# Performance work log

Measured on AMD Instinct MI355X. Metric: run time of the kernel, lower is better.

The kernel has to match this reference:

```python
import jax, jax.numpy as jnp
import numpy as np

B = 32           # graphs in batch
N_PER = 512      # nodes per graph
N = B * N_PER    # 16384 total nodes (block-diagonal batched graph)
E = N * 16       # 262144 edges
D_IN = 128
D_OUT = 128
ASSIGN = 2048    # total clusters = B * K
K = ASSIGN // B  # 64 clusters per graph


def setup_inputs() -> dict:
    key = jax.random.key(0)
    ks = jax.random.split(key, 6)
    h = jax.random.normal(ks[0], (N, D_IN), jnp.float32)
    # edges confined within each graph -> block-diagonal batched adjacency
    gid = jnp.repeat(jnp.arange(B), E // B)
    edge_src = (jax.random.randint(ks[1], (E,), 0, N_PER) + gid * N_PER).astype(jnp.int32)
    edge_dst = (jax.random.randint(ks[2], (E,), 0, N_PER) + gid * N_PER).astype(jnp.int32)
    # GraphSage NodeApply linears: Linear(2*in, out)
    stdv_f = 1.0 / np.sqrt(2 * D_IN)
    W_feat = jax.random.uniform(ks[3], (2 * D_IN, D_OUT), jnp.float32, -stdv_f, stdv_f)
    b_feat = jnp.zeros((D_OUT,), jnp.float32)
    W_pool = jax.random.uniform(ks[4], (2 * D_IN, ASSIGN), jnp.float32, -stdv_f, stdv_f)
    b_pool = jnp.zeros((ASSIGN,), jnp.float32)
    return {"h": h, "W_feat": W_feat, "b_feat": b_feat,
            "W_pool": W_pool, "b_pool": b_pool,
            "edge_src": edge_src, "edge_dst": edge_dst}


def _graphsage(h, W, b, src, dst):
    # mean aggregation over in-neighbors (dropout=0, batch_norm off)
    msg = jax.ops.segment_sum(h[src], dst, num_segments=N)          # [N, d_in]
    deg = jax.ops.segment_sum(jnp.ones((src.shape[0],), h.dtype), dst, num_segments=N)
    h_neigh = msg / jnp.maximum(deg, 1.0)[:, None]
    bundle = jnp.concatenate([h, h_neigh], axis=1) @ W + b          # [N, d_out]
    # F.normalize(p=2, dim=1) then activation, as in GraphSage NodeApply
    norm = jnp.linalg.norm(bundle, axis=1, keepdims=True)
    bundle = bundle / jnp.maximum(norm, 1e-12)
    return jax.nn.relu(bundle)


def _forward(h, W_feat, b_feat, W_pool, b_pool, src, dst):
    feat = _graphsage(h, W_feat, b_feat, src, dst)       # [N, D_OUT]
    assign = _graphsage(h, W_pool, b_pool, src, dst)     # [N, ASSIGN]
    # block-diagonal mask: node i of graph g may only assign to g's K clusters
    gid_n = jnp.arange(N) // N_PER                       # [N]
    gid_c = jnp.arange(ASSIGN) // K                      # [ASSIGN]
    mask = (gid_n[:, None] == gid_c[None, :]).astype(jnp.float32)
    # masked_softmax with memory_efficient=False
    s = jax.nn.softmax(assign * mask, axis=-1) * mask
    s = s / (s.sum(axis=-1, keepdims=True) + 1e-13)      # [N, ASSIGN]
    h_new = s.T @ feat                                   # [ASSIGN, D_OUT]
    # adj_new = S^T A S without densifying A: (A S)[dst] += S[src]
    a_s = jax.ops.segment_sum(s[src], dst, num_segments=N)
    adj_new = s.T @ a_s                                  # [ASSIGN, ASSIGN]
    return adj_new, h_new


def reference(h, W_feat, b_feat, W_pool, b_pool, edge_src, edge_dst):
    return _forward(h, W_feat, b_feat, W_pool, b_pool, edge_src, edge_dst)
```

## Files before the change

### kernel.cpp

```cpp
#include <hip/hip_runtime.h>

#define NB   32
#define NPER 512
#define NN   16384
#define EE   262144
#define DD   128
#define AS   2048
#define KC   64

using short8   = __attribute__((ext_vector_type(8))) short;
using floatx4  = __attribute__((ext_vector_type(4))) float;
using ushort4v = __attribute__((ext_vector_type(4))) unsigned short;

typedef __attribute__((address_space(3))) unsigned int lds_u32;
typedef const __attribute__((address_space(1))) unsigned int gbl_u32;

static __device__ __forceinline__ void gload16(const unsigned short* g, unsigned short* l) {
    __builtin_amdgcn_global_load_lds((gbl_u32*)g, (lds_u32*)l, 16, 0, 0);
}
static __device__ __forceinline__ float bits2f(unsigned int u) {
    union { unsigned int i; float f; } z; z.i = u << 16; return z.f;
}
static __device__ __forceinline__ unsigned short f2b(float x) {
    union { float f; unsigned int u; } v; v.f = x;
    unsigned int r = v.u + 0x7fffu + ((v.u >> 16) & 1u);
    return (unsigned short)(r >> 16);
}
static __device__ __forceinline__ unsigned short f2b_exact(float x) {
    union { float f; unsigned int u; } v; v.f = x;
    return (unsigned short)(v.u >> 16);
}

union PrepSMem {
    unsigned short fT[128 * 136];
    float tl[32][33];
    struct { unsigned short glA[4096]; unsigned short glB[4096]; float gcred[4]; } gg;
};
__global__ void prep_kernel(const float* __restrict__ h, unsigned short* __restrict__ bundle,
                            unsigned short* __restrict__ hT, const int* __restrict__ esrc,
                            const int* __restrict__ edst, unsigned int* __restrict__ Acnt,
                            const float* __restrict__ Wf, const float* __restrict__ Wp,
                            const float* __restrict__ bp,
                            unsigned short* __restrict__ WfT, unsigned short* __restrict__ WpT,
                            float* __restrict__ Gf, float* __restrict__ uF,
                            float* __restrict__ cF) {
    __shared__ PrepSMem sm;
    int b = blockIdx.x, t = threadIdx.x;
    if (b < 32) {
        int ks = b >> 2, ti = (b >> 1) & 1, tj = b & 1;
        int wv = t >> 6, lane = t & 63;
        int mw = wv >> 1, nw = wv & 1, q = lane >> 4, lm = lane & 15;
        int swz = q ^ ((lm >> 1) & 3);
        floatx4 acc[4][4];
#pragma unroll
        for (int mi = 0; mi < 4; mi++)
#pragma unroll
            for (int ni = 0; ni < 4; ni++) acc[mi][ni] = (floatx4)0.f;
        for (int ki = 0; ki < 8; ki++) {
            int k0 = ks * 256 + ki * 32;
#pragma unroll
            for (int half = 0; half < 2; half++) {
                int u = t + 256 * half;
                int row = u >> 2, c = u & 3;
                int cs = c ^ ((row >> 1) & 3);
                const float4* sa = reinterpret_cast<const float4*>(
                    Wp + (size_t)(ti * 128 + row) * 2048 + k0 + c * 8);
                float4 v0 = sa[0], v1 = sa[1];
                ushort4v p0 = { f2b(v0.x), f2b(v0.y), f2b(v0.z), f2b(v0.w) };
                ushort4v p1 = { f2b(v1.x), f2b(v1.y), f2b(v1.z), f2b(v1.w) };
                *reinterpret_cast<ushort4v*>(&sm.gg.glA[(row * 4 + cs) * 8]) = p0;
                *reinterpret_cast<ushort4v*>(&sm.gg.glA[(row * 4 + cs) * 8 + 4]) = p1;
                const float4* sb = reinterpret_cast<const float4*>(
                    Wp + (size_t)(tj * 128 + row) * 2048 + k0 + c * 8);
                float4 w0 = sb[0], w1 = sb[1];
                ushort4v q0 = { f2b(w0.x), f2b(w0.y), f2b(w0.z), f2b(w0.w) };
                ushort4v q1 = { f2b(w1.x), f2b(w1.y), f2b(w1.z), f2b(w1.w) };
                *reinterpret_cast<ushort4v*>(&sm.gg.glB[(row * 4 + cs) * 8]) = q0;
                *reinterpret_cast<ushort4v*>(&sm.gg.glB[(row * 4 + cs) * 8 + 4]) = q1;
            }
            __syncthreads();
            short8 aF[4], bF[4];
#pragma unroll
            for (int mi = 0; mi < 4; mi++)
                aF[mi] = *reinterpret_cast<const short8*>(&sm.gg.glA[((64 * mw + 16 * mi + lm) * 4 + swz) * 8]);
#pragma unroll
            for (int ni = 0; ni < 4; ni++)
                bF[ni] = *reinterpret_cast<const short8*>(&sm.gg.glB[((64 * nw + 16 * ni + lm) * 4 + swz) * 8]);
#pragma unroll
            for (int mi = 0; mi < 4; mi++)
#pragma unroll
                for (int ni = 0; ni < 4; ni++)
                    acc[mi][ni] = __builtin_amdgcn_mfma_f32_16x16x32_bf16(aF[mi], bF[ni], acc[mi][ni], 0, 0, 0);
            __syncthreads();
        }
#pragma unroll
        for (int mi = 0; mi < 4; mi++)
#pragma unroll
            for (int ni = 0; ni < 4; ni++)
#pragma unroll
                for (int r = 0; r < 4; r++)
                    atomicAdd(&Gf[(size_t)(ti * 128 + 64 * mw + 16 * mi + 4 * q + r) * 256 +
                                  tj * 128 + 64 * nw + 16 * ni + lm], acc[mi][ni][r]);
        if (tj == 0) {
            int row = t >> 1, jh = t & 1;
            const float4* wr = reinterpret_cast<const float4*>(
                Wp + (size_t)(ti * 128 + row) * 2048 + ks * 256 + jh * 128);
            const float4* br = reinterpret_cast<const float4*>(bp + ks * 256 + jh * 128);
            float s = 0.f;
#pragma unroll 8
            for (int j = 0; j < 32; j++) {
                float4 a = wr[j], c = br[j];
                s += a.x * c.x + a.y * c.y + a.z * c.z + a.w * c.w;
            }
            s += __shfl_xor(s, 1, 64);
            if (jh == 0) atomicAdd(&uF[ti * 128 + row], s);
        }
        if (b == 0) {
            float s = 0.f;
            for (int j = t; j < 2048; j += 256) { float v = bp[j]; s += v * v; }
#pragma unroll
            for (int d = 1; d < 64; d <<= 1) s += __shfl_xor(s, d, 64);
            if (lane == 0) sm.gg.gcred[wv] = s;
            __syncthreads();
            if (t == 0) atomicAdd(cF, sm.gg.gcred[0] + sm.gg.gcred[1] + sm.gg.gcred[2] + sm.gg.gcred[3]);
        }
    } else if (b < 160) {
        int node0 = (b - 32) * 128;
        int r = t >> 1, hf = t & 1;
        const float4* h4 = reinterpret_cast<const float4*>(h + (size_t)(node0 + r) * 128 + hf * 64);
        unsigned short* bo = bundle + (size_t)(node0 + r) * 256 + hf * 64;
#pragma unroll
        for (int i = 0; i < 16; i++) {
            float4 v = h4[i];
            ushort4v o = { f2b(v.x), f2b(v.y), f2b(v.z), f2b(v.w) };
            *reinterpret_cast<ushort4v*>(bo + 4 * i) = o;
            int c = hf * 64 + 4 * i;
            sm.fT[(c + 0) * 136 + r] = o.x;
            sm.fT[(c + 1) * 136 + r] = o.y;
            sm.fT[(c + 2) * 136 + r] = o.z;
            sm.fT[(c + 3) * 136 + r] = o.w;
        }
        __syncthreads();
        int c = t >> 1, nh = t & 1;
        const uint4* src = reinterpret_cast<const uint4*>(&sm.fT[c * 136 + nh * 64]);
        uint4* dst = reinterpret_cast<uint4*>(hT + (size_t)c * NN + node0 + nh * 64);
#pragma unroll
        for (int i = 0; i < 8; i++) dst[i] = src[i];
    } else if (b < 1184) {
        int e = (b - 160) * 256 + t;
        int d = edst[e], sl = esrc[e] & 511;
        int idx = d * 512 + sl;
        atomicAdd(&Acnt[idx >> 2], 1u << (8 * (idx & 3)));
    } else {
        int tb = b - 1184;
        int bx = tb % 68, by = tb / 68;
        int tx = t & 31, ty = t >> 5;
        const float* in; unsigned short* out; int C, cb;
        if (bx < DD / 32) { in = Wf; out = WfT; C = DD; cb = bx; }
        else              { in = Wp; out = WpT; C = AS; cb = bx - DD / 32; }
        int c0 = cb * 32, r0 = by * 32;
        for (int i = 0; i < 4; i++)
            sm.tl[ty + 8 * i][tx] = in[(size_t)(r0 + ty + 8 * i) * C + c0 + tx];
        __syncthreads();
        for (int i = 0; i < 4; i++)
            out[(size_t)(c0 + ty + 8 * i) * 256 + r0 + tx] = f2b(sm.tl[tx][ty + 8 * i]);
    }
}

__global__ __launch_bounds__(256) void agg_h_mfma_kernel(
    const unsigned int* __restrict__ Acnt, const unsigned short* __restrict__ hT,
    unsigned short* __restrict__ bundle, unsigned short* __restrict__ Aadj,
    const float* __restrict__ Gf, unsigned short* __restrict__ Gb) {
    __shared__ alignas(16) unsigned short lA[64 * 512];
    __shared__ float rs[64];
    int tid = threadIdx.x, bx = blockIdx.x;
    if (bx >= 256) {
        int base = (bx - 256) * 16384;
        for (int i = 0; i < 16; i++) {
            int idx = base + i * 1024 + tid * 4;
            float4 v = *reinterpret_cast<const float4*>(Gf + idx);
            ushort4v o = { f2b(v.x), f2b(v.y), f2b(v.z), f2b(v.w) };
            *reinterpret_cast<ushort4v*>(&Gb[idx]) = o;
        }
        return;
    }
    int r0 = bx * 64, g = bx >> 3;
    int wv = tid >> 6, lane = tid & 63, q = lane >> 4, lm = lane & 15;
    int mw = wv >> 1, nw = wv & 1;
    if (tid < 64) rs[tid] = 0.f;
    __syncthreads();
#pragma unroll
    for (int j = 0; j < 8; j++) {
        int ub = tid + 256 * j;
        int row = ub >> 5, kb = ub & 31;
        uint4 w = reinterpret_cast<const uint4*>(Acnt)[(size_t)(r0 + row) * 32 + kb];
        unsigned int wa[4] = { w.x, w.y, w.z, w.w };
        unsigned short ob[16];
        float sum = 0.f;
#pragma unroll
        for (int i = 0; i < 4; i++) {
#pragma unroll
            for (int bb = 0; bb < 4; bb++) {
                float fv = (float)((wa[i] >> (8 * bb)) & 0xffu);
                sum += fv;
                ob[4 * i + bb] = f2b_exact(fv);
            }
        }
        atomicAdd(&rs[row], sum);
        uint4* gdst = reinterpret_cast<uint4*>(&Aadj[(size_t)(r0 + row) * 512 + kb * 16]);
        gdst[0] = *reinterpret_cast<const uint4*>(&ob[0]);
        gdst[1] = *reinterpret_cast<const uint4*>(&ob[8]);
#pragma unroll
        for (int jj = 0; jj < 2; jj++) {
            int pos = (kb * 2 + jj) ^ (row & 7);
            *reinterpret_cast<uint4*>(&lA[(row * 64 + pos) * 8]) =
                *reinterpret_cast<const uint4*>(&ob[8 * jj]);
        }
    }
    floatx4 acc[2][4];
#pragma unroll
    for (int mt = 0; mt < 2; mt++)
#pragma unroll
        for (int nt = 0; nt < 4; nt++) acc[mt][nt] = (floatx4)0.f;
    __syncthreads();
    const unsigned short* Bb = hT + (size_t)(64 * nw + lm) * NN + g * 512 + (q << 3);
    short8 bF[2][4];
#pragma unroll
    for (int nt = 0; nt < 4; nt++)
        bF[0][nt] = *reinterpret_cast<const short8*>(Bb + (size_t)16 * nt * NN);
    for (int ki = 0; ki < 16; ki++) {
        if (ki < 15) {
#pragma unroll
            for (int nt = 0; nt < 4; nt++)
                bF[(ki + 1) & 1][nt] =
                    *reinterpret_cast<const short8*>(Bb + (size_t)16 * nt * NN + (ki + 1) * 32);
        }
        short8 aF[2];
        int swz = (4 * ki + q) ^ (lm & 7);
#pragma unroll
        for (int mt = 0; mt < 2; mt++)
            aF[mt] = *reinterpret_cast<const short8*>(&lA[((32 * mw + 16 * mt + lm) * 64 + swz) * 8]);
#pragma unroll
        for (int mt = 0; mt < 2; mt++)
#pragma unroll
            for (int nt = 0; nt < 4; nt++)
                acc[mt][nt] = __builtin_amdgcn_mfma_f32_16x16x32_bf16(aF[mt], bF[ki & 1][nt],
                                                                      acc[mt][nt], 0, 0, 0);
    }
#pragma unroll
    for (int mt = 0; mt < 2; mt++)
#pragma unroll
        for (int r = 0; r < 4; r++) {
            int row = 32 * mw + 16 * mt + 4 * q + r;
            float inv = 1.0f / fmaxf(rs[row], 1.0f);
#pragma unroll
            for (int nt = 0; nt < 4; nt++)
                bundle[(size_t)(r0 + row) * 256 + 128 + 64 * nw + 16 * nt + lm] =
                    f2b(acc[mt][nt][r] * inv);
        }
}

union FPSMem {
    struct { unsigned short lA[4096]; unsigned short lB[4096]; float red[256]; } feat;
    struct { unsigned short lA[16384]; float raw[4352]; float ssq[256]; float rn[64];
             float uL[256]; } pool;
};
__global__ __launch_bounds__(256) void featpool_kernel(
    const unsigned short* __restrict__ bundle, const unsigned short* __restrict__ WfT,
    const unsigned short* __restrict__ WpT, const unsigned short* __restrict__ Gb,
    const float* __restrict__ bfe, const float* __restrict__ bp,
    const float* __restrict__ uF, const float* __restrict__ cF,
    unsigned short* __restrict__ featT, unsigned short* __restrict__ sT) {
    __shared__ FPSMem sm;
    int tid = threadIdx.x, b = blockIdx.x;
    if (b < 128) {
        int r0 = b * 128;
        int wv = tid >> 6, lane = tid & 63;
        int mw = wv >> 1, nw = wv & 1, q = lane >> 4, lm = lane & 15;
        int rowS0 = tid >> 2,         cS0 = (tid & 3) ^ ((rowS0 >> 1) & 3);
        int rowS1 = (tid + 256) >> 2, cS1 = ((tid + 256) & 3) ^ ((rowS1 >> 1) & 3);
        int swz = q ^ ((lm >> 1) & 3);
        floatx4 acc[4][4];
#pragma unroll
        for (int mi = 0; mi < 4; mi++)
#pragma unroll
            for (int ni = 0; ni < 4; ni++) acc[mi][ni] = (floatx4)0.f;
        for (int k0 = 0; k0 < 256; k0 += 32) {
            gload16(bundle + (size_t)(r0 + rowS0) * 256 + k0 + 8 * cS0, &sm.feat.lA[tid * 8]);
            gload16(bundle + (size_t)(r0 + rowS1) * 256 + k0 + 8 * cS1, &sm.feat.lA[(tid + 256) * 8]);
            gload16(WfT + (size_t)rowS0 * 256 + k0 + 8 * cS0, &sm.feat.lB[tid * 8]);
            gload16(WfT + (size_t)rowS1 * 256 + k0 + 8 * cS1, &sm.feat.lB[(tid + 256) * 8]);
            __syncthreads();
            short8 aF[4], bF[4];
#pragma unroll
            for (int mi = 0; mi < 4; mi++)
                aF[mi] = *reinterpret_cast<const short8*>(&sm.feat.lA[((64 * mw + 16 * mi + lm) * 4 + swz) * 8]);
#pragma unroll
            for (int ni = 0; ni < 4; ni++)
                bF[ni] = *reinterpret_cast<const short8*>(&sm.feat.lB[((64 * nw + 16 * ni + lm) * 4 + swz) * 8]);
#pragma unroll
            for (int mi = 0; mi < 4; mi++)
#pragma unroll
                for (int ni = 0; ni < 4; ni++)
                    acc[mi][ni] = __builtin_amdgcn_mfma_f32_16x16x32_bf16(aF[mi], bF[ni], acc[mi][ni], 0, 0, 0);
            __syncthreads();
        }
#pragma unroll
        for (int ni = 0; ni < 4; ni++) {
            float bv = bfe[64 * nw + 16 * ni + lm];
#pragma unroll
            for (int mi = 0; mi < 4; mi++)
#pragma unroll
                for (int r = 0; r < 4; r++) acc[mi][ni][r] += bv;
        }
#pragma unroll
        for (int mi = 0; mi < 4; mi++)
#pragma unroll
            for (int r = 0; r < 4; r++) {
                float p = 0.f;
#pragma unroll
                for (int ni = 0; ni < 4; ni++) p += acc[mi][ni][r] * acc[mi][ni][r];
                p += __shfl_xor(p, 1, 64);
                p += __shfl_xor(p, 2, 64);
                p += __shfl_xor(p, 4, 64);
                p += __shfl_xor(p, 8, 64);
                if (lm == 0) sm.feat.red[nw * 128 + 64 * mw + 16 * mi + 4 * q + r] = p;
            }
        __syncthreads();
#pragma unroll
        for (int mi = 0; mi < 4; mi++) {
            float rrn[4];
#pragma unroll
            for (int r = 0; r < 4; r++) {
                int rl = 64 * mw + 16 * mi + 4 * q + r;
                rrn[r] = 1.0f / fmaxf(sqrtf(sm.feat.red[rl] + sm.feat.red[128 + rl]), 1e-12f);
            }
#pragma unroll
            for (int ni = 0; ni < 4; ni++) {
                int col = 64 * nw + 16 * ni + lm;
                ushort4v pk = { f2b(fmaxf(acc[mi][ni][0] * rrn[0], 0.f)),
                                f2b(fmaxf(acc[mi][ni][1] * rrn[1], 0.f)),
                                f2b(fmaxf(acc[mi][ni][2] * rrn[2], 0.f)),
                                f2b(fmaxf(acc[mi][ni][3] * rrn[3], 0.f)) };
                *reinterpret_cast<ushort4v*>(
                    &featT[(size_t)col * NN + r0 + 64 * mw + 16 * mi + 4 * q]) = pk;
            }
        }
    } else {
        int bx = b - 128;
        int r0 = bx * 64, g = bx >> 3;
        int wv = tid >> 6, lane = tid & 63, q = lane >> 4, lm = lane & 15;
#pragma unroll
        for (int j = 0; j < 8; j++) {
            int u = tid + 256 * j;
            int row = u >> 5;
            int chunk = (u & 31) ^ (row & 7);
            gload16(bundle + (size_t)(r0 + row) * 256 + chunk * 8, &sm.pool.lA[u * 8]);
        }
        sm.pool.uL[tid] = uF[tid];
        __syncthreads();
        {
            const unsigned short* Bb = Gb + ((size_t)(wv * 64 + lm) << 8) + (q << 3);
            short8 bF[2][4];
#pragma unroll
            for (int ni = 0; ni < 4; ni++)
                bF[0][ni] = *reinterpret_cast<const short8*>(Bb + (ni << 12));
            floatx4 acc[4][4];
#pragma unroll
            for (int mi = 0; mi < 4; mi++)
#pragma unroll
                for (int ni = 0; ni < 4; ni++) acc[mi][ni] = (floatx4)0.f;
#pragma unroll
            for (int k = 0; k < 8; k++) {
                if (k < 7) {
#pragma unroll
                    for (int ni = 0; ni < 4; ni++)
                        bF[(k + 1) & 1][ni] =
                            *reinterpret_cast<const short8*>(Bb + (ni << 12) + ((k + 1) << 5));
                }
                short8 aF[4];
                int swz = (4 * k + q) ^ (lm & 7);
#pragma unroll
                for (int mi = 0; mi < 4; mi++)
                    aF[mi] = *reinterpret_cast<const short8*>(&sm.pool.lA[((16 * mi + lm) * 32 + swz) * 8]);
#pragma unroll
                for (int mi = 0; mi < 4; mi++)
#pragma unroll
                    for (int ni = 0; ni < 4; ni++)
                        acc[mi][ni] = __builtin_amdgcn_mfma_f32_16x16x32_bf16(aF[mi], bF[k & 1][ni],
                                                                              acc[mi][ni], 0, 0, 0);
            }
            float uc[4];
#pragma unroll
            for (int ni = 0; ni < 4; ni++) uc[ni] = sm.pool.uL[64 * wv + 16 * ni + lm];
#pragma unroll
            for (int mi = 0; mi < 4; mi++)
#pragma unroll
                for (int r = 0; r < 4; r++) {
                    int row = 16 * mi + 4 * q + r;
                    float p = 0.f;
#pragma unroll
                    for (int ni = 0; ni < 4; ni++) {
                        int col = 64 * wv + 16 * ni + lm;
                        int cu = (col >> 3) ^ (row & 7);
                        float xv = bits2f((unsigned int)sm.pool.lA[(row * 32 + cu) * 8 + (col & 7)]);
                        p += (acc[mi][ni][r] + 2.f * uc[ni]) * xv;
                    }
                    p += __shfl_xor(p, 1, 64);
                    p += __shfl_xor(p, 2, 64);
                    p += __shfl_xor(p, 4, 64);
                    p += __shfl_xor(p, 8, 64);
                    if (lm == 0) sm.pool.ssq[wv * 64 + row] = p;
                }
        }
        {
            const unsigned short* Bb2 = WpT + (size_t)(g * KC + 16 * wv + lm) * 256 + (q << 3);
            short8 b2[2];
            b2[0] = *reinterpret_cast<const short8*>(Bb2);
            floatx4 acc2[4];
#pragma unroll
            for (int mi = 0; mi < 4; mi++) acc2[mi] = (floatx4)0.f;
#pragma unroll
            for (int k = 0; k < 8; k++) {
                if (k < 7) b2[(k + 1) & 1] = *reinterpret_cast<const short8*>(Bb2 + ((k + 1) << 5));
                short8 aF[4];
                int swz = (4 * k + q) ^ (lm & 7);
#pragma unroll
                for (int mi = 0; mi < 4; mi++)
                    aF[mi] = *reinterpret_cast<const short8*>(&sm.pool.lA[((16 * mi + lm) * 32 + swz) * 8]);
#pragma unroll
                for (int mi = 0; mi < 4; mi++)
                    acc2[mi] = __builtin_amdgcn_mfma_f32_16x16x32_bf16(aF[mi], b2[k & 1], acc2[mi], 0, 0, 0);
            }
            float bv = bp[g * KC + 16 * wv + lm];
#pragma unroll
            for (int mi = 0; mi < 4; mi++)
#pragma unroll
                for (int r = 0; r < 4; r++)
                    sm.pool.raw[(16 * mi + 4 * q + r) * 68 + 16 * wv + lm] = acc2[mi][r] + bv;
        }
        __syncthreads();
        if (tid < 64)
            sm.pool.rn[tid] = 1.0f / fmaxf(sqrtf(sm.pool.ssq[tid] + sm.pool.ssq[64 + tid] +
                                           sm.pool.ssq[128 + tid] + sm.pool.ssq[192 + tid] + cF[0]), 1e-12f);
        __syncthreads();
        {
            int row = tid >> 2, j = tid & 3;
            int nloc = ((bx & 7) << 6) + row;
            float rn = sm.pool.rn[row];
            float v[16];
            float mx = -1e30f;
#pragma unroll
            for (int c4 = 0; c4 < 4; c4++) {
                float4 rv = *reinterpret_cast<const float4*>(&sm.pool.raw[row * 68 + 16 * j + 4 * c4]);
                v[4 * c4 + 0] = fmaxf(rv.x * rn, 0.f);
                v[4 * c4 + 1] = fmaxf(rv.y * rn, 0.f);
                v[4 * c4 + 2] = fmaxf(rv.z * rn, 0.f);
                v[4 * c4 + 3] = fmaxf(rv.w * rn, 0.f);
            }
#pragma unroll
            for (int c = 0; c < 16; c++) mx = fmaxf(mx, v[c]);
            mx = fmaxf(mx, __shfl_xor(mx, 1, 64));
            mx = fmaxf(mx, __shfl_xor(mx, 2, 64));
            float z = 0.f;
#pragma unroll
            for (int c = 0; c < 16; c++) { v[c] = __expf(v[c] - mx); z += v[c]; }
            z += __shfl_xor(z, 1, 64);
            z += __shfl_xor(z, 2, 64);
            float iz = 1.0f / z;
#pragma unroll
            for (int c4 = 0; c4 < 4; c4++) {
                size_t tb = (size_t)(g * KC + 16 * j + 4 * c4) * NPER + nloc;
                sT[tb] = f2b(v[4 * c4 + 0] * iz);
                sT[tb + NPER] = f2b(v[4 * c4 + 1] * iz);
                sT[tb + 2 * NPER] = f2b(v[4 * c4 + 2] * iz);
                sT[tb + 3 * NPER] = f2b(v[4 * c4 + 3] * iz);
            }
        }
    }
}

__global__ __launch_bounds__(256) void as_mfma_kernel(
    const unsigned short* __restrict__ sT, const unsigned short* __restrict__ Aadj,
    unsigned short* __restrict__ asT) {
    __shared__ alignas(16) unsigned short lS[64 * 512];
    int tid = threadIdx.x, bx = blockIdx.x;
    int g = bx >> 1, half = bx & 1;
    int wv = tid >> 6, lane = tid & 63, q = lane >> 4, lm = lane & 15;
#pragma unroll
    for (int j = 0; j < 16; j++) {
        int u = tid + 256 * j;
        int row = u >> 6, cu = (u & 63) ^ (row & 7);
        gload16(sT + (size_t)(g * KC + row) * NPER + cu * 8, &lS[u * 8]);
    }
    floatx4 acc[4][4];
#pragma unroll
    for (int mi = 0; mi < 4; mi++)
#pragma unroll
        for (int nt = 0; nt < 4; nt++) acc[mi][nt] = (floatx4)0.f;
    __syncthreads();
    int dbase = half * 256 + wv * 64;
    const unsigned short* Bb = Aadj + (size_t)(g * 512 + dbase + lm) * 512 + (q << 3);
    short8 bF[2][4];
#pragma unroll
    for (int nt = 0; nt < 4; nt++)
        bF[0][nt] = *reinterpret_cast<const short8*>(Bb + (size_t)16 * nt * 512);
    for (int ki = 0; ki < 16; ki++) {
        if (ki < 15) {
#pragma unroll
            for (int nt = 0; nt < 4; nt++)
                bF[(ki + 1) & 1][nt] =
                    *reinterpret_cast<const short8*>(Bb + (size_t)16 * nt * 512 + (ki + 1) * 32);
        }
        short8 aF[4];
        int swz = (4 * ki + q) ^ (lm & 7);
#pragma unroll
        for (int mi = 0; mi < 4; mi++)
            aF[mi] = *reinterpret_cast<const short8*>(&lS[((16 * mi + lm) * 64 + swz) * 8]);
#pragma unroll
        for (int mi = 0; mi < 4; mi++)
#pragma unroll
            for (int nt = 0; nt < 4; nt++)
                acc[mi][nt] = __builtin_amdgcn_mfma_f32_16x16x32_bf16(aF[mi], bF[ki & 1][nt],
                                                                      acc[mi][nt], 0, 0, 0);
    }
#pragma unroll
    for (int mi = 0; mi < 4; mi++)
#pragma unroll
        for (int r = 0; r < 4; r++) {
            int row = 16 * mi + 4 * q + r;
#pragma unroll
            for (int nt = 0; nt < 4; nt++)
                asT[(size_t)(g * KC + row) * NPER + dbase + 16 * nt + lm] = f2b(acc[mi][nt][r]);
        }
}

__global__ __launch_bounds__(256) void hnew_adj2_kernel(
    const unsigned short* __restrict__ sT, const unsigned short* __restrict__ featT,
    const unsigned short* __restrict__ asT, float* __restrict__ adjf,
    float* __restrict__ hnewf) {
    __shared__ alignas(16) unsigned short lS[1024 * 8];
    __shared__ alignas(16) unsigned short lF[2048 * 8];
    __shared__ alignas(16) unsigned short lAS[1024 * 8];
    int tid = threadIdx.x, b = blockIdx.x;
    if (b >= 32) {
        uint4 z = { 0u, 0u, 0u, 0u };
        for (int row = b - 32; row < AS; row += 224) {
            int g = row >> 6;
            uint4* out = reinterpret_cast<uint4*>(adjf + (size_t)row * AS);
            for (int i = tid; i < 512; i += 256)
                if (i < g * 16 || i >= g * 16 + 16) out[i] = z;
        }
        return;
    }
    int g = b;
    int wv = tid >> 6, lane = tid & 63, q = lane >> 4, lm = lane & 15;
    bool isH = (wv < 2);
    floatx4 accH[4][4];
    floatx4 accA[4][2];
#pragma unroll
    for (int mi = 0; mi < 4; mi++) {
#pragma unroll
        for (int ni = 0; ni < 4; ni++) accH[mi][ni] = (floatx4)0.f;
#pragma unroll
        for (int ni = 0; ni < 2; ni++) accA[mi][ni] = (floatx4)0.f;
    }
    for (int ks = 0; ks < 4; ks++) {
#pragma unroll
        for (int j = 0; j < 4; j++) {
            int u = tid + 256 * j;
            int row = u >> 4, cu = (u & 15) ^ (row & 15);
            gload16(sT + (size_t)(g * KC + row) * NPER + ks * 128 + cu * 8, &lS[u * 8]);
        }
#pragma unroll
        for (int j = 0; j < 8; j++) {
            int u = tid + 256 * j;
            int row = u >> 4, cu = (u & 15) ^ (row & 15);
            gload16(featT + (size_t)row * NN + g * NPER + ks * 128 + cu * 8, &lF[u * 8]);
        }
#pragma unroll
        for (int j = 0; j < 4; j++) {
            int u = tid + 256 * j;
            int row = u >> 4, cu = (u & 15) ^ (row & 15);
            gload16(asT + (size_t)(g * KC + row) * NPER + ks * 128 + cu * 8, &lAS[u * 8]);
        }
        __syncthreads();
#pragma unroll
        for (int kk = 0; kk < 4; kk++) {
            short8 aF[4];
#pragma unroll
            for (int mi = 0; mi < 4; mi++)
                aF[mi] = *reinterpret_cast<const short8*>(
                    &lS[((16 * mi + lm) * 16 + ((4 * kk + q) ^ lm)) * 8]);
            if (isH) {
                short8 bF[4];
#pragma unroll
                for (int ni = 0; ni < 4; ni++)
                    bF[ni] = *reinterpret_cast<const short8*>(
                        &lF[((64 * wv + 16 * ni + lm) * 16 + ((4 * kk + q) ^ lm)) * 8]);
#pragma unroll
                for (int mi = 0; mi < 4; mi++)
#pragma unroll
                    for (int ni = 0; ni < 4; ni++)
                        accH[mi][ni] = __builtin_amdgcn_mfma_f32_16x16x32_bf16(aF[mi], bF[ni],
                                                                               accH[mi][ni], 0, 0, 0);
            } else {
                short8 bF[2];
#pragma unroll
                for (int ni = 0; ni < 2; ni++)
                    bF[ni] = *reinterpret_cast<const short8*>(
                        &lAS[((32 * (wv - 2) + 16 * ni + lm) * 16 + ((4 * kk + q) ^ lm)) * 8]);
#pragma unroll
                for (int mi = 0; mi < 4; mi++)
#pragma unroll
                    for (int ni = 0; ni < 2; ni++)
                        accA[mi][ni] = __builtin_amdgcn_mfma_f32_16x16x32_bf16(aF[mi], bF[ni],
                                                                               accA[mi][ni], 0, 0, 0);
            }
        }
        __syncthreads();
    }
    if (isH) {
#pragma unroll
        for (int mi = 0; mi < 4; mi++)
#pragma unroll
            for (int ni = 0; ni < 4; ni++)
#pragma unroll
                for (int r = 0; r < 4; r++)
                    hnewf[(size_t)(g * KC + 16 * mi + 4 * q + r) * DD +
                          64 * wv + 16 * ni + lm] = accH[mi][ni][r];
    } else {
#pragma unroll
        for (int mi = 0; mi < 4; mi++)
#pragma unroll
            for (int ni = 0; ni < 2; ni++)
#pragma unroll
                for (int r = 0; r < 4; r++)
                    adjf[(size_t)(g * KC + 16 * mi + 4 * q + r) * AS +
                         g * KC + 32 * (wv - 2) + 16 * ni + lm] = accA[mi][ni][r];
    }
}

extern "C" void kernel_launch(void* const* d_in, const int* in_sizes, int n_in,
                              void* d_out, int out_size, void* d_ws, size_t ws_size,
                              hipStream_t stream) {
    const float* h   = (const float*)d_in[0];
    const float* Wf  = (const float*)d_in[1];
    const float* bfe = (const float*)d_in[2];
    const float* Wp  = (const float*)d_in[3];
    const float* bp  = (const float*)d_in[4];
    const int* esrc  = (const int*)d_in[5];
    const int* edst  = (const int*)d_in[6];

    float* adjf  = (float*)d_out;
    float* hnewf = adjf + (size_t)AS * AS;

    unsigned short* bundle = (unsigned short*)d_ws;
    unsigned short* WfT   = bundle + (size_t)NN * 256;
    unsigned short* WpT   = WfT + 128 * 256;
    unsigned short* sT    = WpT + (size_t)AS * 256;
    unsigned short* asT   = sT + (size_t)NN * KC;
    unsigned short* featT = asT + (size_t)NN * KC;
    unsigned short* hT    = featT + (size_t)DD * NN;
    unsigned short* Aadj  = hT + (size_t)DD * NN;
    unsigned int* Acnt = (unsigned int*)(Aadj + (size_t)NN * 512);
    float* Gf = (float*)(Acnt + (size_t)NN * 128);
    float* uF = Gf + 65536;
    float* cF = uF + 256;
    unsigned short* Gb = (unsigned short*)(cF + 4);

    hipMemsetAsync(Acnt, 0, (size_t)NN * 512 + (65536 + 256 + 4) * sizeof(float), stream);

    prep_kernel<<<1728, 256, 0, stream>>>(h, bundle, hT, esrc, edst, Acnt,
                                          Wf, Wp, bp, WfT, WpT, Gf, uF, cF);
    agg_h_mfma_kernel<<<260, 256, 0, stream>>>(Acnt, hT, bundle, Aadj, Gf, Gb);
    featpool_kernel<<<384, 256, 0, stream>>>(bundle, WfT, WpT, Gb, bfe, bp, uF, cF, featT, sT);
    as_mfma_kernel<<<NB * 2, 256, 0, stream>>>(sT, Aadj, asT);
    hnew_adj2_kernel<<<256, 256, 0, stream>>>(sT, featT, asT, adjf, hnewf);
}
```

Baseline: 162.9 us.

## Fuse neighbor aggregation, feature linear and pool softmax into one mid kernel

Merges the aggregation MFMA kernel and the feat/pool linear kernel into a single per-64-row block kernel. The aggregated half of each bundle row stays in LDS instead of round-tripping through global memory. The Gram matrix is converted to bf16 in registers on the fly, which removes the separate Gf-to-Gb conversion blocks. Row degree sums now use wave shuffles instead of LDS atomics. The cost is fewer blocks (256 instead of 384+260) with a larger LDS footprint, and serialized phases per block, which may lower occupancy and parallelism.

```diff
diff --git a/kernel.cpp b/kernel.cpp
--- a/kernel.cpp
+++ b/kernel.cpp
@@ -1,4 +1,5 @@
 #include <hip/hip_runtime.h>
+#include <hip/hip_bf16.h>
 
 #define NB   32
 #define NPER 512
@@ -29,6 +30,18 @@
 static __device__ __forceinline__ unsigned short f2b_exact(float x) {
     union { float f; unsigned int u; } v; v.f = x;
     return (unsigned short)(v.u >> 16);
+}
+static __device__ __forceinline__ short8 pk8(float4 a, float4 b) {
+    union { short8 s; unsigned int u[4]; } o;
+    __hip_bfloat162 t0 = __float22bfloat162_rn(make_float2(a.x, a.y));
+    __hip_bfloat162 t1 = __float22bfloat162_rn(make_float2(a.z, a.w));
+    __hip_bfloat162 t2 = __float22bfloat162_rn(make_float2(b.x, b.y));
+    __hip_bfloat162 t3 = __float22bfloat162_rn(make_float2(b.z, b.w));
+    o.u[0] = *reinterpret_cast<unsigned int*>(&t0);
+    o.u[1] = *reinterpret_cast<unsigned int*>(&t1);
+    o.u[2] = *reinterpret_cast<unsigned int*>(&t2);
+    o.u[3] = *reinterpret_cast<unsigned int*>(&t3);
+    return o.s;
 }
 
 union PrepSMem {
@@ -167,28 +180,33 @@
     }
 }
 
-__global__ __launch_bounds__(256) void agg_h_mfma_kernel(
+union MSMem {
+    unsigned short lA[64 * 512];
+    struct {
+        unsigned short tile[64 * 256];
+        float rs[64];
+        float raw[64 * 68];
+        float ssq[256];
+        float rn[64];
+        float uL[256];
+        float red[256];
+        float rn2[64];
+    } p;
+};
+__global__ __launch_bounds__(256) void fused_mid_kernel(
     const unsigned int* __restrict__ Acnt, const unsigned short* __restrict__ hT,
-    unsigned short* __restrict__ bundle, unsigned short* __restrict__ Aadj,
-    const float* __restrict__ Gf, unsigned short* __restrict__ Gb) {
-    __shared__ alignas(16) unsigned short lA[64 * 512];
-    __shared__ float rs[64];
+    const unsigned short* __restrict__ bundle, unsigned short* __restrict__ Aadj,
+    const float* __restrict__ Gf, const unsigned short* __restrict__ WpT,
+    const unsigned short* __restrict__ WfT, const float* __restrict__ bfe,
+    const float* __restrict__ bp, const float* __restrict__ uF, const float* __restrict__ cF,
+    unsigned short* __restrict__ featT, unsigned short* __restrict__ sT) {
+    __shared__ MSMem sm;
     int tid = threadIdx.x, bx = blockIdx.x;
-    if (bx >= 256) {
-        int base = (bx - 256) * 16384;
-        for (int i = 0; i < 16; i++) {
-            int idx = base + i * 1024 + tid * 4;
-            float4 v = *reinterpret_cast<const float4*>(Gf + idx);
-            ushort4v o = { f2b(v.x), f2b(v.y), f2b(v.z), f2b(v.w) };
-            *reinterpret_cast<ushort4v*>(&Gb[idx]) = o;
-        }
-        return;
-    }
     int r0 = bx * 64, g = bx >> 3;
     int wv = tid >> 6, lane = tid & 63, q = lane >> 4, lm = lane & 15;
     int mw = wv >> 1, nw = wv & 1;
-    if (tid < 64) rs[tid] = 0.f;
-    __syncthreads();
+
+    float rsum[8];
 #pragma unroll
     for (int j = 0; j < 8; j++) {
         int ub = tid + 256 * j;
@@ -206,16 +224,21 @@
                 ob[4 * i + bb] = f2b_exact(fv);
             }
         }
-        atomicAdd(&rs[row], sum);
         uint4* gdst = reinterpret_cast<uint4*>(&Aadj[(size_t)(r0 + row) * 512 + kb * 16]);
         gdst[0] = *reinterpret_cast<const uint4*>(&ob[0]);
         gdst[1] = *reinterpret_cast<const uint4*>(&ob[8]);
 #pragma unroll
         for (int jj = 0; jj < 2; jj++) {
             int pos = (kb * 2 + jj) ^ (row & 7);
-            *reinterpret_cast<uint4*>(&lA[(row * 64 + pos) * 8]) =
+            *reinterpret_cast<uint4*>(&sm.lA[(row * 64 + pos) * 8]) =
                 *reinterpret_cast<const uint4*>(&ob[8 * jj]);
         }
+        sum += __shfl_xor(sum, 1, 64);
+        sum += __shfl_xor(sum, 2, 64);
+        sum += __shfl_xor(sum, 4, 64);
+        sum += __shfl_xor(sum, 8, 64);
+        sum += __shfl_xor(sum, 16, 64);
+        rsum[j] = sum;
     }
     floatx4 acc[2][4];
 #pragma unroll
@@ -223,258 +246,270 @@
 #pragma unroll
         for (int nt = 0; nt < 4; nt++) acc[mt][nt] = (floatx4)0.f;
     __syncthreads();
-    const unsigned short* Bb = hT + (size_t)(64 * nw + lm) * NN + g * 512 + (q << 3);
-    short8 bF[2][4];
-#pragma unroll
-    for (int nt = 0; nt < 4; nt++)
-        bF[0][nt] = *reinterpret_cast<const short8*>(Bb + (size_t)16 * nt * NN);
-    for (int ki = 0; ki < 16; ki++) {
-        if (ki < 15) {
-#pragma unroll
-            for (int nt = 0; nt < 4; nt++)
-                bF[(ki + 1) & 1][nt] =
-                    *reinterpret_cast<const short8*>(Bb + (size_t)16 * nt * NN + (ki + 1) * 32);
-        }
-        short8 aF[2];
-        int swz = (4 * ki + q) ^ (lm & 7);
-#pragma unroll
-        for (int mt = 0; mt < 2; mt++)
-            aF[mt] = *reinterpret_cast<const short8*>(&lA[((32 * mw + 16 * mt + lm) * 64 + swz) * 8]);
-#pragma unroll
-        for (int mt = 0; mt < 2; mt++)
-#pragma unroll
-            for (int nt = 0; nt < 4; nt++)
-                acc[mt][nt] = __builtin_amdgcn_mfma_f32_16x16x32_bf16(aF[mt], bF[ki & 1][nt],
-                                                                      acc[mt][nt], 0, 0, 0);
-    }
+    {
+        const unsigned short* Bb = hT + (size_t)(64 * nw + lm) * NN + g * 512 + (q << 3);
+        short8 bF[2][4];
+#pragma unroll
+        for (int nt = 0; nt < 4; nt++)
+            bF[0][nt] = *reinterpret_cast<const short8*>(Bb + (size_t)16 * nt * NN);
+        for (int ki = 0; ki < 16; ki++) {
+            if (ki < 15) {
+#pragma unroll
+                for (int nt = 0; nt < 4; nt++)
+                    bF[(ki + 1) & 1][nt] =
+                        *reinterpret_cast<const short8*>(Bb + (size_t)16 * nt * NN + (ki + 1) * 32);
+            }
+            short8 aF[2];
+            int swz = (4 * ki + q) ^ (lm & 7);
+#pragma unroll
+            for (int mt = 0; mt < 2; mt++)
+                aF[mt] = *reinterpret_cast<const short8*>(&sm.lA[((32 * mw + 16 * mt + lm) * 64 + swz) * 8]);
+#pragma unroll
+            for (int mt = 0; mt < 2; mt++)
+#pragma unroll
+                for (int nt = 0; nt < 4; nt++)
+                    acc[mt][nt] = __builtin_amdgcn_mfma_f32_16x16x32_bf16(aF[mt], bF[ki & 1][nt],
+                                                                          acc[mt][nt], 0, 0, 0);
+        }
+    }
+    __syncthreads();
+    if ((tid & 31) == 0) {
+#pragma unroll
+        for (int j = 0; j < 8; j++) sm.p.rs[(tid + 256 * j) >> 5] = rsum[j];
+    }
+#pragma unroll
+    for (int j = 0; j < 4; j++) {
+        int u = tid + 256 * j;
+        int row = u >> 4, c = u & 15;
+        int cg = c ^ (row & 7);
+        gload16(bundle + (size_t)(r0 + row) * 256 + cg * 8, &sm.p.tile[u * 8]);
+    }
+    sm.p.uL[tid] = uF[tid];
+    __syncthreads();
 #pragma unroll
     for (int mt = 0; mt < 2; mt++)
 #pragma unroll
         for (int r = 0; r < 4; r++) {
             int row = 32 * mw + 16 * mt + 4 * q + r;
-            float inv = 1.0f / fmaxf(rs[row], 1.0f);
-#pragma unroll
-            for (int nt = 0; nt < 4; nt++)
-                bundle[(size_t)(r0 + row) * 256 + 128 + 64 * nw + 16 * nt + lm] =
+            float inv = 1.0f / fmaxf(sm.p.rs[row], 1.0f);
+#pragma unroll
+            for (int nt = 0; nt < 4; nt++) {
+                int cloc = 64 * nw + 16 * nt + lm;
+                int sloc = (cloc >> 3) ^ (row & 7);
+                sm.p.tile[8192 + (row * 16 + sloc) * 8 + (cloc & 7)] =
                     f2b(acc[mt][nt][r] * inv);
-        }
-}
-
-union FPSMem {
-    struct { unsigned short lA[4096]; unsigned short lB[4096]; float red[256]; } feat;
-    struct { unsigned short lA[16384]; float raw[4352]; float ssq[256]; float rn[64];
-             float uL[256]; } pool;
-};
-__global__ __launch_bounds__(256) void featpool_kernel(
-    const unsigned short* __restrict__ bundle, const unsigned short* __restrict__ WfT,
-    const unsigned short* __restrict__ WpT, const unsigned short* __restrict__ Gb,
-    const float* __restrict__ bfe, const float* __restrict__ bp,
-    const float* __restrict__ uF, const float* __restrict__ cF,
-    unsigned short* __restrict__ featT, unsigned short* __restrict__ sT) {
-    __shared__ FPSMem sm;
-    int tid = threadIdx.x, b = blockIdx.x;
-    if (b < 128) {
-        int r0 = b * 128;
-        int wv = tid >> 6, lane = tid & 63;
-        int mw = wv >> 1, nw = wv & 1, q = lane >> 4, lm = lane & 15;
-        int rowS0 = tid >> 2,         cS0 = (tid & 3) ^ ((rowS0 >> 1) & 3);
-        int rowS1 = (tid + 256) >> 2, cS1 = ((tid + 256) & 3) ^ ((rowS1 >> 1) & 3);
-        int swz = q ^ ((lm >> 1) & 3);
-        floatx4 acc[4][4];
-#pragma unroll
-        for (int mi = 0; mi < 4; mi++)
-#pragma unroll
-            for (int ni = 0; ni < 4; ni++) acc[mi][ni] = (floatx4)0.f;
-        for (int k0 = 0; k0 < 256; k0 += 32) {
-            gload16(bundle + (size_t)(r0 + rowS0) * 256 + k0 + 8 * cS0, &sm.feat.lA[tid * 8]);
-            gload16(bundle + (size_t)(r0 + rowS1) * 256 + k0 + 8 * cS1, &sm.feat.lA[(tid + 256) * 8]);
-            gload16(WfT + (size_t)rowS0 * 256 + k0 + 8 * cS0, &sm.feat.lB[tid * 8]);
-            gload16(WfT + (size_t)rowS1 * 256 + k0 + 8 * cS1, &sm.feat.lB[(tid + 256) * 8]);
-            __syncthreads();
-            short8 aF[4], bF[4];
-#pragma unroll
-            for (int mi = 0; mi < 4; mi++)
-                aF[mi] = *reinterpret_cast<const short8*>(&sm.feat.lA[((64 * mw + 16 * mi + lm) * 4 + swz) * 8]);
-#pragma unroll
-            for (int ni = 0; ni < 4; ni++)
-                bF[ni] = *reinterpret_cast<const short8*>(&sm.feat.lB[((64 * nw + 16 * ni + lm) * 4 + swz) * 8]);
+            }
+        }
+    __syncthreads();
+
+    {
+        const float* Bf = Gf + (size_t)(64 * wv + lm) * 256 + (q << 3);
+        short8 bF[2][4];
+        float4 tA[4], tB[4];
+#pragma unroll
+        for (int ni = 0; ni < 4; ni++) {
+            tA[ni] = *reinterpret_cast<const float4*>(Bf + (ni << 12));
+            tB[ni] = *reinterpret_cast<const float4*>(Bf + (ni << 12) + 4);
+        }
+#pragma unroll
+        for (int ni = 0; ni < 4; ni++) bF[0][ni] = pk8(tA[ni], tB[ni]);
+        floatx4 pacc[4][4];
+#pragma unroll
+        for (int mi = 0; mi < 4; mi++)
+#pragma unroll
+            for (int ni = 0; ni < 4; ni++) pacc[mi][ni] = (floatx4)0.f;
+#pragma unroll
+        for (int k = 0; k < 8; k++) {
+            if (k < 7) {
+#pragma unroll
+                for (int ni = 0; ni < 4; ni++) {
+                    tA[ni] = *reinterpret_cast<const float4*>(Bf + (ni << 12) + ((k + 1) << 5));
+                    tB[ni] = *reinterpret_cast<const float4*>(Bf + (ni << 12) + ((k + 1) << 5) + 4);
+                }
+            }
+            short8 aF[4];
+            const unsigned short* reg = (k < 4) ? sm.p.tile : (sm.p.tile + 8192);
+            int kk = k & 3;
+#pragma unroll
+            for (int mi = 0; mi < 4; mi++)
+                aF[mi] = *reinterpret_cast<const short8*>(
+                    &reg[((16 * mi + lm) * 16 + ((4 * kk + q) ^ (lm & 7))) * 8]);
 #pragma unroll
             for (int mi = 0; mi < 4; mi++)
 #pragma unroll
                 for (int ni = 0; ni < 4; ni++)
-                    acc[mi][ni] = __builtin_amdgcn_mfma_f32_16x16x32_bf16(aF[mi], bF[ni], acc[mi][ni], 0, 0, 0);
-            __syncthreads();
-        }
-#pragma unroll
-        for (int ni = 0; ni < 4; ni++) {
-            float bv = bfe[64 * nw + 16 * ni + lm];
-#pragma unroll
-            for (int mi = 0; mi < 4; mi++)
-#pragma unroll
-                for (int r = 0; r < 4; r++) acc[mi][ni][r] += bv;
-        }
+                    pacc[mi][ni] = __builtin_amdgcn_mfma_f32_16x16x32_bf16(aF[mi], bF[k & 1][ni],
+                                                                           pacc[mi][ni], 0, 0, 0);
+            if (k < 7) {
+#pragma unroll
+                for (int ni = 0; ni < 4; ni++) bF[(k + 1) & 1][ni] = pk8(tA[ni], tB[ni]);
+            }
+        }
+        float uc[4];
+#pragma unroll
+        for (int ni = 0; ni < 4; ni++) uc[ni] = sm.p.uL[64 * wv + 16 * ni + lm];
+        const unsigned short* regX = (wv < 2) ? sm.p.tile : (sm.p.tile + 8192);
 #pragma unroll
         for (int mi = 0; mi < 4; mi++)
 #pragma unroll
             for (int r = 0; r < 4; r++) {
+                int row = 16 * mi + 4 * q + r;
                 float p = 0.f;
 #pragma unroll
-                for (int ni = 0; ni < 4; ni++) p += acc[mi][ni][r] * acc[mi][ni][r];
+                for (int ni = 0; ni < 4; ni++) {
+                    int cl = (64 * wv + 16 * ni + lm) & 127;
+                    int cu = (cl >> 3) ^ (row & 7);
+                    float xv = bits2f((unsigned int)regX[(row * 16 + cu) * 8 + (cl & 7)]);
+                    p += (pacc[mi][ni][r] + 2.f * uc[ni]) * xv;
+                }
                 p += __shfl_xor(p, 1, 64);
                 p += __shfl_xor(p, 2, 64);
                 p += __shfl_xor(p, 4, 64);
                 p += __shfl_xor(p, 8, 64);
-                if (lm == 0) sm.feat.red[nw * 128 + 64 * mw + 16 * mi + 4 * q + r] = p;
-            }
+                if (lm == 0) sm.p.ssq[wv * 64 + row] = p;
+            }
+    }
+    {
+        const unsigned short* Bb2 = WpT + (size_t)(g * KC + 16 * wv + lm) * 256 + (q << 3);
+        short8 b2[2];
+        b2[0] = *reinterpret_cast<const short8*>(Bb2);
+        floatx4 acc2[4];
+#pragma unroll
+        for (int mi = 0; mi < 4; mi++) acc2[mi] = (floatx4)0.f;
+#pragma unroll
+        for (int k = 0; k < 8; k++) {
+            if (k < 7) b2[(k + 1) & 1] = *reinterpret_cast<const short8*>(Bb2 + ((k + 1) << 5));
+            short8 aF[4];
+            const unsigned short* reg = (k < 4) ? sm.p.tile : (sm.p.tile + 8192);
+            int kk = k & 3;
+#pragma unroll
+            for (int mi = 0; mi < 4; mi++)
+                aF[mi] = *reinterpret_cast<const short8*>(
+                    &reg[((16 * mi + lm) * 16 + ((4 * kk + q) ^ (lm & 7))) * 8]);
+#pragma unroll
+            for (int mi = 0; mi < 4; mi++)
+                acc2[mi] = __builtin_amdgcn_mfma_f32_16x16x32_bf16(aF[mi], b2[k & 1], acc2[mi], 0, 0, 0);
+        }
+        float bv = bp[g * KC + 16 * wv + lm];
+#pragma unroll
+        for (int mi = 0; mi < 4; mi++)
+#pragma unroll
+            for (int r = 0; r < 4; r++)
+                sm.p.raw[(16 * mi + 4 * q + r) * 68 + 16 * wv + lm] = acc2[mi][r] + bv;
+    }
+    __syncthreads();
+    if (tid < 64)
+        sm.p.rn[tid] = 1.0f / fmaxf(sqrtf(sm.p.ssq[tid] + sm.p.ssq[64 + tid] +
+                                    sm.p.ssq[128 + tid] + sm.p.ssq[192 + tid] + cF[0]), 1e-12f);
+    __syncthreads();
+    {
+        int row = tid >> 2, j = tid & 3;
+        int nloc = ((bx & 7) << 6) + row;
+        float rn = sm.p.rn[row];
+        float v[16];
+        float mx = -1e30f;
+#pragma unroll
+        for (int c4 = 0; c4 < 4; c4++) {
+            float4 rv = *reinterpret_cast<const float4*>(&sm.p.raw[row * 68 + 16 * j + 4 * c4]);
+            v[4 * c4 + 0] = fmaxf(rv.x * rn, 0.f);
+            v[4 * c4 + 1] = fmaxf(rv.y * rn, 0.f);
+            v[4 * c4 + 2] = fmaxf(rv.z * rn, 0.f);
+            v[4 * c4 + 3] = fmaxf(rv.w * rn, 0.f);
+        }
+#pragma unroll
+        for (int c = 0; c < 16; c++) mx = fmaxf(mx, v[c]);
+        mx = fmaxf(mx, __shfl_xor(mx, 1, 64));
+        mx = fmaxf(mx, __shfl_xor(mx, 2, 64));
+        float z = 0.f;
+#pragma unroll
+        for (int c = 0; c < 16; c++) { v[c] = __expf(v[c] - mx); z += v[c]; }
+        z += __shfl_xor(z, 1, 64);
+        z += __shfl_xor(z, 2, 64);
+        float iz = 1.0f / z;
+#pragma unroll
+        for (int c4 = 0; c4 < 4; c4++) {
+            size_t tb = (size_t)(g * KC + 16 * j + 4 * c4) * NPER + nloc;
+            sT[tb] = f2b(v[4 * c4 + 0] * iz);
+            sT[tb + NPER] = f2b(v[4 * c4 + 1] * iz);
+            sT[tb + 2 * NPER] = f2b(v[4 * c4 + 2] * iz);
+            sT[tb + 3 * NPER] = f2b(v[4 * c4 + 3] * iz);
+        }
+    }
+    __syncthreads();
+
+    {
+        const unsigned short* Bf2 = WfT + (size_t)(32 * wv + lm) * 256 + (q << 3);
+        short8 bF[2][2];
+#pragma unroll
+        for (int ni = 0; ni < 2; ni++)
+            bF[0][ni] = *reinterpret_cast<const short8*>(Bf2 + (ni << 12));
+        floatx4 facc[4][2];
+#pragma unroll
+        for (int mi = 0; mi < 4; mi++)
+#pragma unroll
+            for (int ni = 0; ni < 2; ni++) facc[mi][ni] = (floatx4)0.f;
+#pragma unroll
+        for (int k = 0; k < 8; k++) {
+            if (k < 7) {
+#pragma unroll
+                for (int ni = 0; ni < 2; ni++)
+                    bF[(k + 1) & 1][ni] =
+                        *reinterpret_cast<const short8*>(Bf2 + (ni << 12) + ((k + 1) << 5));
+            }
+            short8 aF[4];
+            const unsigned short* reg = (k < 4) ? sm.p.tile : (sm.p.tile + 8192);
+            int kk = k & 3;
+#pragma unroll
+            for (int mi = 0; mi < 4; mi++)
+                aF[mi] = *reinterpret_cast<const short8*>(
+                    &reg[((16 * mi + lm) * 16 + ((4 * kk + q) ^ (lm & 7))) * 8]);
+#pragma unroll
+            for (int mi = 0; mi < 4; mi++)
+#pragma unroll
+                for (int ni = 0; ni < 2; ni++)
+                    facc[mi][ni] = __builtin_amdgcn_mfma_f32_16x16x32_bf16(aF[mi], bF[k & 1][ni],
+                                                                           facc[mi][ni], 0, 0, 0);
+        }
+#pragma unroll
+        for (int ni = 0; ni < 2; ni++) {
+            float bv = bfe[32 * wv + 16 * ni + lm];
+#pragma unroll
+            for (int mi = 0; mi < 4; mi++)
+#pragma unroll
+                for (int r = 0; r < 4; r++) facc[mi][ni][r] += bv;
+        }
+#pragma unroll
+        for (int mi = 0; mi < 4; mi++)
+#pragma unroll
+            for (int r = 0; r < 4; r++) {
+                float p = 0.f;
+#pragma unroll
+                for (int ni = 0; ni < 2; ni++) p += facc[mi][ni][r] * facc[mi][ni][r];
+                p += __shfl_xor(p, 1, 64);
+                p += __shfl_xor(p, 2, 64);
+                p += __shfl_xor(p, 4, 64);
+                p += __shfl_xor(p, 8, 64);
+                if (lm == 0) sm.p.red[wv * 64 + 16 * mi + 4 * q + r] = p;
+            }
+        __syncthreads();
+        if (tid < 64)
+            sm.p.rn2[tid] = 1.0f / fmaxf(sqrtf(sm.p.red[tid] + sm.p.red[64 + tid] +
+                                         sm.p.red[128 + tid] + sm.p.red[192 + tid]), 1e-12f);
         __syncthreads();
 #pragma unroll
         for (int mi = 0; mi < 4; mi++) {
             float rrn[4];
 #pragma unroll
-            for (int r = 0; r < 4; r++) {
-                int rl = 64 * mw + 16 * mi + 4 * q + r;
-                rrn[r] = 1.0f / fmaxf(sqrtf(sm.feat.red[rl] + sm.feat.red[128 + rl]), 1e-12f);
-            }
-#pragma unroll
-            for (int ni = 0; ni < 4; ni++) {
-                int col = 64 * nw + 16 * ni + lm;
-                ushort4v pk = { f2b(fmaxf(acc[mi][ni][0] * rrn[0], 0.f)),
-                                f2b(fmaxf(acc[mi][ni][1] * rrn[1], 0.f)),
-                                f2b(fmaxf(acc[mi][ni][2] * rrn[2], 0.f)),
-                                f2b(fmaxf(acc[mi][ni][3] * rrn[3], 0.f)) };
+            for (int r = 0; r < 4; r++) rrn[r] = sm.p.rn2[16 * mi + 4 * q + r];
+#pragma unroll
+            for (int ni = 0; ni < 2; ni++) {
+                int col = 32 * wv + 16 * ni + lm;
+                ushort4v pk = { f2b(fmaxf(facc[mi][ni][0] * rrn[0], 0.f)),
+                                f2b(fmaxf(facc[mi][ni][1] * rrn[1], 0.f)),
+                                f2b(fmaxf(facc[mi][ni][2] * rrn[2], 0.f)),
+                                f2b(fmaxf(facc[mi][ni][3] * rrn[3], 0.f)) };
                 *reinterpret_cast<ushort4v*>(
-                    &featT[(size_t)col * NN + r0 + 64 * mw + 16 * mi + 4 * q]) = pk;
-            }
-        }
-    } else {
-        int bx = b - 128;
-        int r0 = bx * 64, g = bx >> 3;
-        int wv = tid >> 6, lane = tid & 63, q = lane >> 4, lm = lane & 15;
-#pragma unroll
-        for (int j = 0; j < 8; j++) {
-            int u = tid + 256 * j;
-            int row = u >> 5;
-            int chunk = (u & 31) ^ (row & 7);
-            gload16(bundle + (size_t)(r0 + row) * 256 + chunk * 8, &sm.pool.lA[u * 8]);
-        }
-        sm.pool.uL[tid] = uF[tid];
-        __syncthreads();
-        {
-            const unsigned short* Bb = Gb + ((size_t)(wv * 64 + lm) << 8) + (q << 3);
-            short8 bF[2][4];
-#pragma unroll
-            for (int ni = 0; ni < 4; ni++)
-                bF[0][ni] = *reinterpret_cast<const short8*>(Bb + (ni << 12));
-            floatx4 acc[4][4];
-#pragma unroll
-            for (int mi = 0; mi < 4; mi++)
-#pragma unroll
-                for (int ni = 0; ni < 4; ni++) acc[mi][ni] = (floatx4)0.f;
-#pragma unroll
-            for (int k = 0; k < 8; k++) {
-                if (k < 7) {
-#pragma unroll
-                    for (int ni = 0; ni < 4; ni++)
-                        bF[(k + 1) & 1][ni] =
-                            *reinterpret_cast<const short8*>(Bb + (ni << 12) + ((k + 1) << 5));
-                }
-                short8 aF[4];
-                int swz = (4 * k + q) ^ (lm & 7);
-#pragma unroll
-                for (int mi = 0; mi < 4; mi++)
-                    aF[mi] = *reinterpret_cast<const short8*>(&sm.pool.lA[((16 * mi + lm) * 32 + swz) * 8]);
-#pragma unroll
-                for (int mi = 0; mi < 4; mi++)
-#pragma unroll
-                    for (int ni = 0; ni < 4; ni++)
-                        acc[mi][ni] = __builtin_amdgcn_mfma_f32_16x16x32_bf16(aF[mi], bF[k & 1][ni],
-                                                                              acc[mi][ni], 0, 0, 0);
-            }
-            float uc[4];
-#pragma unroll
-            for (int ni = 0; ni < 4; ni++) uc[ni] = sm.pool.uL[64 * wv + 16 * ni + lm];
-#pragma unroll
-            for (int mi = 0; mi < 4; mi++)
-#pragma unroll
-                for (int r = 0; r < 4; r++) {
-                    int row = 16 * mi + 4 * q + r;
-                    float p = 0.f;
-#pragma unroll
-                    for (int ni = 0; ni < 4; ni++) {
-                        int col = 64 * wv + 16 * ni + lm;
-                        int cu = (col >> 3) ^ (row & 7);
-                        float xv = bits2f((unsigned int)sm.pool.lA[(row * 32 + cu) * 8 + (col & 7)]);
-                        p += (acc[mi][ni][r] + 2.f * uc[ni]) * xv;
-                    }
-                    p += __shfl_xor(p, 1, 64);
-                    p += __shfl_xor(p, 2, 64);
-                    p += __shfl_xor(p, 4, 64);
-                    p += __shfl_xor(p, 8, 64);
-                    if (lm == 0) sm.pool.ssq[wv * 64 + row] = p;
-                }
-        }
-        {
-            const unsigned short* Bb2 = WpT + (size_t)(g * KC + 16 * wv + lm) * 256 + (q << 3);
-            short8 b2[2];
-            b2[0] = *reinterpret_cast<const short8*>(Bb2);
-            floatx4 acc2[4];
-#pragma unroll
-            for (int mi = 0; mi < 4; mi++) acc2[mi] = (floatx4)0.f;
-#pragma unroll
-            for (int k = 0; k < 8; k++) {
-                if (k < 7) b2[(k + 1) & 1] = *reinterpret_cast<const short8*>(Bb2 + ((k + 1) << 5));
-                short8 aF[4];
-                int swz = (4 * k + q) ^ (lm & 7);
-#pragma unroll
-                for (int mi = 0; mi < 4; mi++)
-                    aF[mi] = *reinterpret_cast<const short8*>(&sm.pool.lA[((16 * mi + lm) * 32 + swz) * 8]);
-#pragma unroll
-                for (int mi = 0; mi < 4; mi++)
-                    acc2[mi] = __builtin_amdgcn_mfma_f32_16x16x32_bf16(aF[mi], b2[k & 1], acc2[mi], 0, 0, 0);
-            }
-            float bv = bp[g * KC + 16 * wv + lm];
-#pragma unroll
-            for (int mi = 0; mi < 4; mi++)
-#pragma unroll
-                for (int r = 0; r < 4; r++)
-                    sm.pool.raw[(16 * mi + 4 * q + r) * 68 + 16 * wv + lm] = acc2[mi][r] + bv;
-        }
-        __syncthreads();
-        if (tid < 64)
-            sm.pool.rn[tid] = 1.0f / fmaxf(sqrtf(sm.pool.ssq[tid] + sm.pool.ssq[64 + tid] +
-                                           sm.pool.ssq[128 + tid] + sm.pool.ssq[192 + tid] + cF[0]), 1e-12f);
-        __syncthreads();
-        {
-            int row = tid >> 2, j = tid & 3;
-            int nloc = ((bx & 7) << 6) + row;
-            float rn = sm.pool.rn[row];
-            float v[16];
-            float mx = -1e30f;
-#pragma unroll
-            for (int c4 = 0; c4 < 4; c4++) {
-                float4 rv = *reinterpret_cast<const float4*>(&sm.pool.raw[row * 68 + 16 * j + 4 * c4]);
-                v[4 * c4 + 0] = fmaxf(rv.x * rn, 0.f);
-                v[4 * c4 + 1] = fmaxf(rv.y * rn, 0.f);
-                v[4 * c4 + 2] = fmaxf(rv.z * rn, 0.f);
-                v[4 * c4 + 3] = fmaxf(rv.w * rn, 0.f);
-            }
-#pragma unroll
-            for (int c = 0; c < 16; c++) mx = fmaxf(mx, v[c]);
-            mx = fmaxf(mx, __shfl_xor(mx, 1, 64));
-            mx = fmaxf(mx, __shfl_xor(mx, 2, 64));
-            float z = 0.f;
-#pragma unroll
-            for (int c = 0; c < 16; c++) { v[c] = __expf(v[c] - mx); z += v[c]; }
-            z += __shfl_xor(z, 1, 64);
-            z += __shfl_xor(z, 2, 64);
-            float iz = 1.0f / z;
-#pragma unroll
-            for (int c4 = 0; c4 < 4; c4++) {
-                size_t tb = (size_t)(g * KC + 16 * j + 4 * c4) * NPER + nloc;
-                sT[tb] = f2b(v[4 * c4 + 0] * iz);
-                sT[tb + NPER] = f2b(v[4 * c4 + 1] * iz);
-                sT[tb + 2 * NPER] = f2b(v[4 * c4 + 2] * iz);
-                sT[tb + 3 * NPER] = f2b(v[4 * c4 + 3] * iz);
+                    &featT[(size_t)col * NN + r0 + 16 * mi + 4 * q]) = pk;
             }
         }
     }
@@ -667,14 +702,13 @@
     float* Gf = (float*)(Acnt + (size_t)NN * 128);
     float* uF = Gf + 65536;
     float* cF = uF + 256;
-    unsigned short* Gb = (unsigned short*)(cF + 4);
 
     hipMemsetAsync(Acnt, 0, (size_t)NN * 512 + (65536 + 256 + 4) * sizeof(float), stream);
 
     prep_kernel<<<1728, 256, 0, stream>>>(h, bundle, hT, esrc, edst, Acnt,
                                           Wf, Wp, bp, WfT, WpT, Gf, uF, cF);
-    agg_h_mfma_kernel<<<260, 256, 0, stream>>>(Acnt, hT, bundle, Aadj, Gf, Gb);
-    featpool_kernel<<<384, 256, 0, stream>>>(bundle, WfT, WpT, Gb, bfe, bp, uF, cF, featT, sT);
+    fused_mid_kernel<<<256, 256, 0, stream>>>(Acnt, hT, bundle, Aadj, Gf, WpT, WfT,
+                                              bfe, bp, uF, cF, featT, sT);
     as_mfma_kernel<<<NB * 2, 256, 0, stream>>>(sT, Aadj, asT);
     hnew_adj2_kernel<<<256, 256, 0, stream>>>(sT, featT, asT, adjf, hnewf);
 }
```

Result: no change. 165.0 us (+1.3%).
